# Kernel optimization log

Hardware: AMD Instinct MI355X
Metric: run time of the kernel (lower is better)

## Reference

```python
import jax, jax.numpy as jnp
import numpy as np

N_L = 128
N_R = 128
VOCAB = 50000
IN_DIM = 512
MEM = 256
HID = 128
NCLS = 5


def _make_parents(n, seed):
    # children-before-parent topological order: parent[i] > i, root = n-1 with sentinel parent n
    rng = np.random.RandomState(seed)
    p = np.array([rng.randint(i + 1, n) if i < n - 1 else n for i in range(n)], dtype=np.int32)
    return jnp.asarray(p)


def setup_inputs() -> dict:
    key = jax.random.key(0)
    ks = jax.random.split(key, 18)
    s = 0.05
    inp = {
        'emb': jax.random.normal(ks[0], (VOCAB, IN_DIM), jnp.float32) * 0.1,
        'Wioux': jax.random.normal(ks[1], (IN_DIM, 3 * MEM), jnp.float32) * s,
        'bioux': jnp.zeros((3 * MEM,), jnp.float32),
        'Wiouh': jax.random.normal(ks[2], (MEM, 3 * MEM), jnp.float32) * s,
        'biouh': jnp.zeros((3 * MEM,), jnp.float32),
        'Wfx': jax.random.normal(ks[3], (IN_DIM, MEM), jnp.float32) * s,
        'bfx': jnp.zeros((MEM,), jnp.float32),
        'Wfh': jax.random.normal(ks[4], (MEM, MEM), jnp.float32) * s,
        'bfh': jnp.zeros((MEM,), jnp.float32),
        'Wattn': jax.random.normal(ks[5], (2 * MEM, MEM), jnp.float32) * s,
        'battn': jnp.zeros((MEM,), jnp.float32),
        'Wwh': jax.random.normal(ks[6], (2 * MEM, HID), jnp.float32) * s,
        'bwh': jnp.zeros((HID,), jnp.float32),
        'Wwp': jax.random.normal(ks[7], (HID, NCLS), jnp.float32) * s,
        'bwp': jnp.zeros((NCLS,), jnp.float32),
        'linputs': jax.random.randint(ks[8], (N_L,), 0, VOCAB, jnp.int32),
        'lparents': _make_parents(N_L, 11),
        'rinputs': jax.random.randint(ks[9], (N_R,), 0, VOCAB, jnp.int32),
        'rparents': _make_parents(N_R, 13),
    }
    return inp


def _tree_lstm(X, parents, Wioux, bioux, Wiouh, biouh, Wfx, bfx, Wfh, bfh):
    # X: [N, in_dim]; parents: [N] int, parent index > node index, root's parent == N (sentinel)
    N = X.shape[0]
    m = Wfh.shape[0]
    ioux_all = X @ Wioux + bioux          # [N, 3m] precomputed input contribution
    fx_all = X @ Wfx + bfx                # [N, m]
    fx_pad = jnp.concatenate([fx_all, jnp.zeros((1, m), X.dtype)], axis=0)  # sentinel row

    def step(carry, t):
        Hs, FCs, H = carry                # accumulators: sum of child h / forget-gated child c
        iou = ioux_all[t] + Hs[t] @ Wiouh + biouh
        i_, o_, u_ = jnp.split(iou, 3)
        i_ = jax.nn.sigmoid(i_)
        o_ = jax.nn.sigmoid(o_)
        u_ = jnp.tanh(u_)
        c = i_ * u_ + FCs[t]
        h = o_ * jnp.tanh(c)
        p = parents[t]
        f = jax.nn.sigmoid(h @ Wfh + bfh + fx_pad[p])  # forget gate of this child at its parent
        return (Hs.at[p].add(h), FCs.at[p].add(f * c), H.at[t].set(h)), None

    init = (jnp.zeros((N + 1, m), X.dtype), jnp.zeros((N + 1, m), X.dtype), jnp.zeros((N, m), X.dtype))
    (_, _, H), _ = jax.lax.scan(step, init, jnp.arange(N))
    return H


def reference(emb, Wioux, bioux, Wiouh, biouh, Wfx, bfx, Wfh, bfh,
              Wattn, battn, Wwh, bwh, Wwp, bwp,
              linputs, lparents, rinputs, rparents):
    Xl = emb[linputs]
    Xr = emb[rinputs]
    Hl = _tree_lstm(Xl, lparents, Wioux, bioux, Wiouh, biouh, Wfx, bfx, Wfh, bfh)  # [Nl, m]
    Hr = _tree_lstm(Xr, rparents, Wioux, bioux, Wiouh, biouh, Wfx, bfx, Wfh, bfh)  # [Nr, m]

    S = Hl @ Hr.T                                      # [Nl, Nr]
    beta_sum = jax.nn.softmax(S, axis=1) @ Hr          # [Nl, m]
    alpha_sum = jax.nn.softmax(S.T, axis=1) @ Hl       # [Nr, m]

    v_l = jnp.concatenate([Hl, beta_sum], axis=1) @ Wattn + battn
    v_r = jnp.concatenate([Hr, alpha_sum], axis=1) @ Wattn + battn

    lh = v_l[Hl.shape[0] - 1][None, :]                 # root of left tree
    rh = v_r[Hr.shape[0] - 1][None, :]                 # root of right tree

    vec = jnp.concatenate([lh * rh, jnp.abs(lh - rh)], axis=1)
    out = jax.nn.sigmoid(vec @ Wwh + bwh)
    return jax.nn.log_softmax(out @ Wwp + bwp, axis=1)
```

## Files before the change

### kernel.cpp

```cpp
#include <hip/hip_runtime.h>
#include <math.h>

typedef unsigned long long ull;

#define H_BYTE     0
#define IOUX_BYTE  262144
#define FLAG_BYTE  1310720

__device__ __forceinline__ float sigmf(float x){ return 1.0f/(1.0f+__expf(-x)); }
__device__ __forceinline__ float tanh_fast(float x){ float e=__expf(2.0f*x); return 1.0f-2.0f/(e+1.0f); }

__device__ __forceinline__ ull aload64(const ull* p){
    return __hip_atomic_load(p, __ATOMIC_RELAXED, __HIP_MEMORY_SCOPE_AGENT);
}
__device__ __forceinline__ float aloadf(const float* p){
    return __hip_atomic_load(p, __ATOMIC_RELAXED, __HIP_MEMORY_SCOPE_AGENT);
}
__device__ __forceinline__ void astoref(float* p, float v){
    __hip_atomic_store(p, v, __ATOMIC_RELAXED, __HIP_MEMORY_SCOPE_AGENT);
}
__device__ __forceinline__ int aload32(const int* p){
    return __hip_atomic_load(p, __ATOMIC_RELAXED, __HIP_MEMORY_SCOPE_AGENT);
}
__device__ __forceinline__ void astore32(int* p, int v){
    __hip_atomic_store(p, v, __ATOMIC_RELAXED, __HIP_MEMORY_SCOPE_AGENT);
}

__global__ __launch_bounds__(256) void k1_gemm(
        const float* __restrict__ emb,
        const float* __restrict__ Wioux, const float* __restrict__ bioux,
        const float* __restrict__ Wfx,   const float* __restrict__ bfx,
        const int* __restrict__ linputs, const int* __restrict__ rinputs,
        float* __restrict__ ws){
    int bid  = blockIdx.x;
    int tree = bid >> 6;
    int sub  = (bid >> 2) & 15;
    int q    = bid & 3;
    int n0   = q * 32;
    const int* inp = tree ? rinputs : linputs;
    float* dst = (float*)((char*)ws + IOUX_BYTE) + (size_t)(tree*16+sub)*128*64;

    __shared__ float Xs[32][513];
    __shared__ int toks[32];
    int tid = threadIdx.x;
    if (tid < 32) toks[tid] = inp[n0 + tid];
    __syncthreads();
    {
        int r = tid & 31, seg = tid >> 5;
        const float* src = emb + (size_t)toks[r]*512 + seg*64;
        #pragma unroll
        for (int ii = 0; ii < 16; ii++){
            float4 v = ((const float4*)src)[ii];
            Xs[r][seg*64 + ii*4 + 0] = v.x;
            Xs[r][seg*64 + ii*4 + 1] = v.y;
            Xs[r][seg*64 + ii*4 + 2] = v.z;
            Xs[r][seg*64 + ii*4 + 3] = v.w;
        }
    }
    __syncthreads();
    int c  = tid & 63;
    int ng = tid >> 6;
    int g = c >> 4, jj = c & 15;
    const float* Wcol; int ld; float bias;
    if (g < 3){ int col = g*256 + sub*16 + jj; Wcol = Wioux + col; ld = 768; bias = bioux[col]; }
    else      { int col = sub*16 + jj;         Wcol = Wfx + col;   ld = 256; bias = bfx[col]; }
    float acc[8] = {0,0,0,0,0,0,0,0};
    #pragma unroll 4
    for (int k = 0; k < 512; k++){
        float w = Wcol[(size_t)k*ld];
        #pragma unroll
        for (int i = 0; i < 8; i++) acc[i] = fmaf(Xs[ng*8+i][k], w, acc[i]);
    }
    #pragma unroll
    for (int i = 0; i < 8; i++)
        dst[(size_t)(n0 + ng*8 + i)*64 + c] = acc[i] + bias;
}

__global__ __launch_bounds__(256, 1) void k2_scan(
        const float* __restrict__ Wiouh, const float* __restrict__ biouh,
        const float* __restrict__ Wfh,   const float* __restrict__ bfh,
        const int* __restrict__ lparents, const int* __restrict__ rparents,
        const float* __restrict__ Wattn, const float* __restrict__ battn,
        const float* __restrict__ Wwh,   const float* __restrict__ bwh,
        const float* __restrict__ Wwp,   const float* __restrict__ bwp,
        float* __restrict__ ws, float* __restrict__ out){

    int bid = blockIdx.x;
    int tree = bid >> 4;
    int sub  = bid & 15;
    int slice = sub * 16;
    const int* parents = tree ? rparents : lparents;

    float* Hall = (float*)((char*)ws + H_BYTE);
    float* Hg   = Hall + (size_t)tree*128*256;
    const float* iosrc = (const float*)((char*)ws + IOUX_BYTE) + (size_t)(tree*16+sub)*128*64;
    int* flagB = (int*)((char*)ws + FLAG_BYTE);
    int* flags = flagB + tree*16;
    int* fin   = flagB + 32;

    __shared__ float hv[32][272];
    __shared__ float hsin[16][272];
    __shared__ float red[4][48][17];
    __shared__ float FCtmp[32][17];
    __shared__ float fcin[16][17];
    __shared__ float cc[128][17];
    __shared__ float ioufL[128][68];
    __shared__ int par[128], rnd[128], order[128], kids[128];
    __shared__ int rstart[129], kstart[129], cnt[129];
    __shared__ int clist[128], cpar[128];
    __shared__ int coff[17];
    __shared__ int changed;

    int tid = threadIdx.x;
    int a = tid >> 4;
    int j = tid & 15;
    int jcol = slice + j;

    float Wi[16], Wo[16], Wu[16], Wf[16];
    #pragma unroll
    for (int kk = 0; kk < 16; kk++){
        int k = a*16 + kk;
        Wi[kk] = Wiouh[(size_t)k*768 + jcol];
        Wo[kk] = Wiouh[(size_t)k*768 + 256 + jcol];
        Wu[kk] = Wiouh[(size_t)k*768 + 512 + jcol];
        Wf[kk] = Wfh[(size_t)k*256 + jcol];
    }
    float bioI = biouh[jcol], bioO = biouh[256+jcol], bioU = biouh[512+jcol];
    float bfv  = bfh[jcol];

    for (int i = tid; i < 128*16; i += 256){
        int n = i >> 4, f4 = i & 15;
        float4 v = ((const float4*)(iosrc + (size_t)n*64))[f4];
        int c0 = f4*4;
        ioufL[n][c0+0]=v.x; ioufL[n][c0+1]=v.y; ioufL[n][c0+2]=v.z; ioufL[n][c0+3]=v.w;
    }

    if (tid < 128){ par[tid] = parents[tid]; rnd[tid] = 0; }
    __syncthreads();
    for(;;){
        if (tid==0) changed = 0;
        __syncthreads();
        if (tid < 128){
            int p = par[tid];
            if (p < 128){
                int v = rnd[tid] + 1;
                if (atomicMax(&rnd[p], v) < v) changed = 1;
            }
        }
        __syncthreads();
        int done = (changed == 0);
        __syncthreads();
        if (done) break;
    }
    int nr = rnd[127] + 1;

    if (tid <= 128) cnt[tid] = 0;
    __syncthreads();
    if (tid < 128) atomicAdd(&cnt[rnd[tid]], 1);
    __syncthreads();
    if (tid==0){ int s2=0; for(int r2=0;r2<128;r2++){ rstart[r2]=s2; s2+=cnt[r2]; } rstart[128]=s2; }
    __syncthreads();
    if (tid < 128){
        int r2 = rnd[tid], rk = 0;
        for (int t2 = 0; t2 < tid; t2++) rk += (rnd[t2]==r2);
        order[rstart[r2]+rk] = tid;
    }
    __syncthreads();
    if (tid <= 128) cnt[tid] = 0;
    __syncthreads();
    if (tid < 128) atomicAdd(&cnt[par[tid]], 1);
    __syncthreads();
    if (tid==0){ int s2=0; for(int t2=0;t2<=128;t2++){ kstart[t2]=s2; s2+=cnt[t2]; } }
    __syncthreads();
    if (tid < 128){
        int p = par[tid], rk = 0;
        for (int t2 = 0; t2 < tid; t2++) rk += (par[t2]==p);
        kids[kstart[p]+rk] = tid;
    }
    __syncthreads();

    for (int r = 0; r < nr; r++){
        if (r > 0){
            if (tid < 16){
                while (aload32(&flags[tid]) < r){}
            }
            __syncthreads();
        }
        int rs = rstart[r], re = rstart[r+1];

        if (r == 0){
            for (int b0 = rs; b0 < re; b0 += 16){
                int t = (b0 + a < re) ? order[b0 + a] : -1;
                if (t >= 0){
                    float iv = ioufL[t][j]    + bioI;
                    float ov = ioufL[t][16+j] + bioO;
                    float uv = ioufL[t][32+j] + bioU;
                    float cv = sigmf(iv) * tanh_fast(uv);
                    float h  = sigmf(ov) * tanh_fast(cv);
                    cc[t][j] = cv;
                    astoref(&Hg[(size_t)t*256 + jcol], h);
                }
            }
        } else {
            for (int b0 = rs; b0 < re; b0 += 16){
                int nn = re - b0; if (nn > 16) nn = 16;
                for (int i = tid; i < 16*272; i += 256) (&hsin[0][0])[i] = 0.f;
                fcin[a][j] = 0.f;
                if (tid == 0){
                    int s2 = 0;
                    for (int i2 = 0; i2 < 16; i2++){
                        coff[i2] = s2;
                        if (i2 < nn){ int t2 = order[b0+i2]; s2 += kstart[t2+1]-kstart[t2]; }
                    }
                    coff[16] = s2;
                }
                __syncthreads();
                if (tid < nn){
                    int t2 = order[b0+tid];
                    int o = coff[tid];
                    for (int ci = kstart[t2]; ci < kstart[t2+1]; ci++, o++){
                        clist[o] = kids[ci]; cpar[o] = t2;
                    }
                }
                __syncthreads();
                int M = coff[16];

                for (int cb = 0; cb < M; cb += 32){
                    int mm = M - cb; if (mm > 32) mm = 32;
                    {
                        int half = tid >> 7, u7 = tid & 127;
                        int k0 = u7*2, km = (k0>>4)*17 + (k0&15);
                        const ull* Hu = (const ull*)Hg;
                        ull uu[8];
                        #pragma unroll
                        for (int p = 0; p < 8; p++){
                            int s = p*2 + half;
                            uu[p] = (s < mm) ? aload64(&Hu[(size_t)clist[cb+s]*128 + u7]) : 0ull;
                        }
                        #pragma unroll
                        for (int p = 0; p < 8; p++){
                            int s = p*2 + half;
                            if (s < mm){ union{ull u; float f[2];} w; w.u = uu[p];
                                hv[s][km] = w.f[0]; hv[s][km+1] = w.f[1]; }
                        }
                        #pragma unroll
                        for (int p = 0; p < 8; p++){
                            int s = (p+8)*2 + half;
                            uu[p] = (s < mm) ? aload64(&Hu[(size_t)clist[cb+s]*128 + u7]) : 0ull;
                        }
                        #pragma unroll
                        for (int p = 0; p < 8; p++){
                            int s = (p+8)*2 + half;
                            if (s < mm){ union{ull u; float f[2];} w; w.u = uu[p];
                                hv[s][km] = w.f[0]; hv[s][km+1] = w.f[1]; }
                        }
                    }
                    __syncthreads();
                    for (int s = 0; s < mm; s++){
                        const float* row = &hv[s][a*17];
                        float acc2 = 0.f;
                        #pragma unroll
                        for (int kk = 0; kk < 16; kk++) acc2 = fmaf(Wf[kk], row[kk], acc2);
                        acc2 += __shfl_xor(acc2, 16);
                        acc2 += __shfl_xor(acc2, 32);
                        if ((a & 3) == 0) red[tid>>6][s][j] = acc2;
                    }
                    __syncthreads();
                    for (int pass = 0; pass*16 < mm; pass++){
                        int s = pass*16 + a;
                        if (s < mm){
                            int o = cb + s;
                            float sf = red[0][s][j]+red[1][s][j]+red[2][s][j]+red[3][s][j];
                            float f = sigmf(sf + bfv + ioufL[cpar[o]][48+j]);
                            FCtmp[s][j] = f * cc[clist[o]][j];
                        }
                    }
                    __syncthreads();
                    {
                        int o0 = coff[a]   > cb    ? coff[a]   : cb;
                        int o1 = coff[a+1] < cb+mm ? coff[a+1] : cb+mm;
                        float* dst = &hsin[a][j*17];
                        float fa = 0.f;
                        for (int o = o0; o < o1; o++){
                            int s = o - cb;
                            const float* src = &hv[s][j*17];
                            #pragma unroll
                            for (int kk = 0; kk < 16; kk++) dst[kk] += src[kk];
                            fa += FCtmp[s][j];
                        }
                        fcin[a][j] += fa;
                    }
                    __syncthreads();
                }

                for (int n = 0; n < nn; n++){
                    const float* row = &hsin[n][a*17];
                    float x=0.f, y=0.f, z=0.f;
                    #pragma unroll
                    for (int kk = 0; kk < 16; kk++){
                        float v = row[kk];
                        x = fmaf(Wi[kk], v, x);
                        y = fmaf(Wo[kk], v, y);
                        z = fmaf(Wu[kk], v, z);
                    }
                    x += __shfl_xor(x,16); x += __shfl_xor(x,32);
                    y += __shfl_xor(y,16); y += __shfl_xor(y,32);
                    z += __shfl_xor(z,16); z += __shfl_xor(z,32);
                    if ((a & 3) == 0){
                        int w = tid >> 6;
                        red[w][n][j]    = x;
                        red[w][16+n][j] = y;
                        red[w][32+n][j] = z;
                    }
                }
                __syncthreads();
                if (a < nn){
                    int t = order[b0+a];
                    float si = red[0][a][j]+red[1][a][j]+red[2][a][j]+red[3][a][j];
                    float so = red[0][16+a][j]+red[1][16+a][j]+red[2][16+a][j]+red[3][16+a][j];
                    float su = red[0][32+a][j]+red[1][32+a][j]+red[2][32+a][j]+red[3][32+a][j];
                    float iv = si + ioufL[t][j]    + bioI;
                    float ov = so + ioufL[t][16+j] + bioO;
                    float uv = su + ioufL[t][32+j] + bioU;
                    float cv = fmaf(sigmf(iv), tanh_fast(uv), fcin[a][j]);
                    float h  = sigmf(ov) * tanh_fast(cv);
                    cc[t][j] = cv;
                    astoref(&Hg[(size_t)t*256 + jcol], h);
                }
                __syncthreads();
            }
        }

        __syncthreads();
        if (tid == 0){
            if (r < nr-1) astore32(&flags[sub], r+1);
            else          astore32(&fin[bid], 1);
        }
    }

    if (bid != 0) return;
    if (tid < 32){
        while (aload32(&fin[tid]) < 1){}
    }
    __syncthreads();

    float* F  = &hv[0][0];
    float* rl = F,        *rr  = F + 256;
    float* sA = F + 512,  *sB  = F + 640;
    float* bet= F + 768,  *alp = F + 1024;
    float* vl = F + 1280, *vr  = F + 1536;
    float* vec= F + 1792, *hid = F + 2304;
    const ull* HuL = (const ull*)Hall;
    const ull* HuR = (const ull*)(Hall + 128*256);

    {
        union{ ull u; float f[2]; } w2;
        if (tid < 128){
            w2.u = aload64(&HuL[(size_t)127*128 + tid]);
            rl[2*tid] = w2.f[0]; rl[2*tid+1] = w2.f[1];
        } else {
            int p = tid - 128;
            w2.u = aload64(&HuR[(size_t)127*128 + p]);
            rr[2*p] = w2.f[0]; rr[2*p+1] = w2.f[1];
        }
    }
    __syncthreads();
    {
        int i = tid & 127;
        const ull* row = (tid < 128) ? &HuR[(size_t)i*128] : &HuL[(size_t)i*128];
        const float* rt = (tid < 128) ? rl : rr;
        float acc2 = 0.f;
        for (int p0 = 0; p0 < 128; p0 += 16){
            ull u[16];
            #pragma unroll
            for (int q2 = 0; q2 < 16; q2++) u[q2] = aload64(&row[p0+q2]);
            #pragma unroll
            for (int q2 = 0; q2 < 16; q2++){
                union{ ull uu; float f[2]; } w2; w2.uu = u[q2];
                acc2 = fmaf(w2.f[0], rt[2*(p0+q2)],   acc2);
                acc2 = fmaf(w2.f[1], rt[2*(p0+q2)+1], acc2);
            }
        }
        if (tid < 128) sA[i] = acc2; else sB[i] = acc2;
    }
    __syncthreads();
    if (tid < 2){
        float* v = tid ? sB : sA;
        float m = -1e30f;
        for (int k = 0; k < 128; k++) m = fmaxf(m, v[k]);
        float su2 = 0.f;
        for (int k = 0; k < 128; k++){ float e = __expf(v[k]-m); v[k]=e; su2+=e; }
        float inv = 1.0f/su2;
        for (int k = 0; k < 128; k++) v[k] *= inv;
    }
    __syncthreads();
    {
        const float* HrF = Hall + 128*256;
        const float* HlF = Hall;
        float b = 0.f, al = 0.f;
        for (int i0 = 0; i0 < 128; i0 += 16){
            float ur[16], ulv[16];
            #pragma unroll
            for (int q2 = 0; q2 < 16; q2++){
                ur[q2]  = aloadf(&HrF[(size_t)(i0+q2)*256 + tid]);
                ulv[q2] = aloadf(&HlF[(size_t)(i0+q2)*256 + tid]);
            }
            #pragma unroll
            for (int q2 = 0; q2 < 16; q2++){
                b  = fmaf(sA[i0+q2], ur[q2],  b);
                al = fmaf(sB[i0+q2], ulv[q2], al);
            }
        }
        bet[tid] = b; alp[tid] = al;
    }
    __syncthreads();
    {
        float x = 0.f, y = 0.f;
        for (int k = 0; k < 256; k++){
            float w = Wattn[(size_t)k*256 + tid];
            x = fmaf(rl[k], w, x);
            y = fmaf(rr[k], w, y);
        }
        for (int k = 0; k < 256; k++){
            float w = Wattn[(size_t)(256+k)*256 + tid];
            x = fmaf(bet[k], w, x);
            y = fmaf(alp[k], w, y);
        }
        vl[tid] = x + battn[tid];
        vr[tid] = y + battn[tid];
    }
    __syncthreads();
    vec[tid]     = vl[tid]*vr[tid];
    vec[256+tid] = fabsf(vl[tid]-vr[tid]);
    __syncthreads();
    if (tid < 128){
        float acc2 = 0.f;
        for (int k = 0; k < 512; k++) acc2 = fmaf(vec[k], Wwh[(size_t)k*128+tid], acc2);
        hid[tid] = sigmf(acc2 + bwh[tid]);
    }
    __syncthreads();
    if (tid == 0){
        float lg[5];
        for (int c2 = 0; c2 < 5; c2++){
            float acc2 = bwp[c2];
            for (int k = 0; k < 128; k++) acc2 = fmaf(hid[k], Wwp[k*5+c2], acc2);
            lg[c2] = acc2;
        }
        float m = lg[0];
        for (int c2 = 1; c2 < 5; c2++) m = fmaxf(m, lg[c2]);
        float su2 = 0.f;
        for (int c2 = 0; c2 < 5; c2++) su2 += __expf(lg[c2]-m);
        float ls = logf(su2);
        for (int c2 = 0; c2 < 5; c2++) out[c2] = lg[c2]-m-ls;
    }
}

extern "C" void kernel_launch(void* const* d_in, const int* in_sizes, int n_in,
                              void* d_out, int out_size, void* d_ws, size_t ws_size,
                              hipStream_t stream) {
    const float* emb    = (const float*)d_in[0];
    const float* Wioux  = (const float*)d_in[1];
    const float* bioux  = (const float*)d_in[2];
    const float* Wiouh  = (const float*)d_in[3];
    const float* biouh  = (const float*)d_in[4];
    const float* Wfx    = (const float*)d_in[5];
    const float* bfx    = (const float*)d_in[6];
    const float* Wfh    = (const float*)d_in[7];
    const float* bfh    = (const float*)d_in[8];
    const float* Wattn  = (const float*)d_in[9];
    const float* battn  = (const float*)d_in[10];
    const float* Wwh    = (const float*)d_in[11];
    const float* bwh    = (const float*)d_in[12];
    const float* Wwp    = (const float*)d_in[13];
    const float* bwp    = (const float*)d_in[14];
    const int* linputs  = (const int*)d_in[15];
    const int* lparents = (const int*)d_in[16];
    const int* rinputs  = (const int*)d_in[17];
    const int* rparents = (const int*)d_in[18];
    float* ws  = (float*)d_ws;
    float* out = (float*)d_out;

    hipMemsetAsync((char*)d_ws + FLAG_BYTE, 0, 256, stream);
    k1_gemm<<<128, 256, 0, stream>>>(emb, Wioux, bioux, Wfx, bfx,
                                     linputs, rinputs, ws);
    k2_scan<<<32, 256, 0, stream>>>(Wiouh, biouh, Wfh, bfh, lparents, rparents,
                                    Wattn, battn, Wwh, bwh, Wwp, bwp, ws, out);
}
```

Baseline: 195.7 us.

## Overlap inter-block wait with processing of children from earlier rounds

```diff
diff --git a/kernel.cpp b/kernel.cpp
--- a/kernel.cpp
+++ b/kernel.cpp
@@ -107,8 +107,8 @@
     __shared__ float ioufL[128][68];
     __shared__ int par[128], rnd[128], order[128], kids[128];
     __shared__ int rstart[129], kstart[129], cnt[129];
-    __shared__ int clist[128], cpar[128];
-    __shared__ int coff[17];
+    __shared__ int clistO[128], cparO[128], clistN[128], cparN[128];
+    __shared__ int coffO[17], coffN[17], cntO[16], cntN[16];
     __shared__ int changed;
 
     int tid = threadIdx.x;
@@ -179,156 +179,183 @@
     }
     __syncthreads();
 
-    for (int r = 0; r < nr; r++){
-        if (r > 0){
+    auto processList = [&](const int* cl, const int* cp, const int* cf){
+        int M = cf[16];
+        for (int cb = 0; cb < M; cb += 32){
+            int mm = M - cb; if (mm > 32) mm = 32;
+            {
+                int half = tid >> 7, u7 = tid & 127;
+                int k0 = u7*2, km = (k0>>4)*17 + (k0&15);
+                const ull* Hu = (const ull*)Hg;
+                ull uu[8];
+                #pragma unroll
+                for (int p = 0; p < 8; p++){
+                    int s = p*2 + half;
+                    uu[p] = (s < mm) ? aload64(&Hu[(size_t)cl[cb+s]*128 + u7]) : 0ull;
+                }
+                #pragma unroll
+                for (int p = 0; p < 8; p++){
+                    int s = p*2 + half;
+                    if (s < mm){ union{ull u; float f[2];} w; w.u = uu[p];
+                        hv[s][km] = w.f[0]; hv[s][km+1] = w.f[1]; }
+                }
+                #pragma unroll
+                for (int p = 0; p < 8; p++){
+                    int s = (p+8)*2 + half;
+                    uu[p] = (s < mm) ? aload64(&Hu[(size_t)cl[cb+s]*128 + u7]) : 0ull;
+                }
+                #pragma unroll
+                for (int p = 0; p < 8; p++){
+                    int s = (p+8)*2 + half;
+                    if (s < mm){ union{ull u; float f[2];} w; w.u = uu[p];
+                        hv[s][km] = w.f[0]; hv[s][km+1] = w.f[1]; }
+                }
+            }
+            __syncthreads();
+            for (int s = 0; s < mm; s++){
+                const float* row = &hv[s][a*17];
+                float acc2 = 0.f;
+                #pragma unroll
+                for (int kk = 0; kk < 16; kk++) acc2 = fmaf(Wf[kk], row[kk], acc2);
+                acc2 += __shfl_xor(acc2, 16);
+                acc2 += __shfl_xor(acc2, 32);
+                if ((a & 3) == 0) red[tid>>6][s][j] = acc2;
+            }
+            __syncthreads();
+            for (int pass = 0; pass*16 < mm; pass++){
+                int s = pass*16 + a;
+                if (s < mm){
+                    int o = cb + s;
+                    float sf = red[0][s][j]+red[1][s][j]+red[2][s][j]+red[3][s][j];
+                    float f = sigmf(sf + bfv + ioufL[cp[o]][48+j]);
+                    FCtmp[s][j] = f * cc[cl[o]][j];
+                }
+            }
+            __syncthreads();
+            {
+                int o0 = cf[a]   > cb    ? cf[a]   : cb;
+                int o1 = cf[a+1] < cb+mm ? cf[a+1] : cb+mm;
+                float* dst = &hsin[a][j*17];
+                float fa = 0.f;
+                for (int o = o0; o < o1; o++){
+                    int s = o - cb;
+                    const float* src = &hv[s][j*17];
+                    #pragma unroll
+                    for (int kk = 0; kk < 16; kk++) dst[kk] += src[kk];
+                    fa += FCtmp[s][j];
+                }
+                fcin[a][j] += fa;
+            }
+            __syncthreads();
+        }
+    };
+
+    {
+        int rs = rstart[0], re = rstart[1];
+        for (int b0 = rs; b0 < re; b0 += 16){
+            int t = (b0 + a < re) ? order[b0 + a] : -1;
+            if (t >= 0){
+                float iv = ioufL[t][j]    + bioI;
+                float ov = ioufL[t][16+j] + bioO;
+                float uv = ioufL[t][32+j] + bioU;
+                float cv = sigmf(iv) * tanh_fast(uv);
+                float h  = sigmf(ov) * tanh_fast(cv);
+                cc[t][j] = cv;
+                astoref(&Hg[(size_t)t*256 + jcol], h);
+            }
+        }
+        __syncthreads();
+        if (tid == 0){
+            if (nr > 1) astore32(&flags[sub], 1);
+            else        astore32(&fin[bid], 1);
+        }
+    }
+
+    for (int r = 1; r < nr; r++){
+        int rs = rstart[r], re = rstart[r+1];
+        int nb = (re - rs + 15) >> 4;
+        for (int b = 0; b < nb; b++){
+            int b0 = rs + b*16;
+            int nn = re - b0; if (nn > 16) nn = 16;
+            for (int i = tid; i < 16*272; i += 256) (&hsin[0][0])[i] = 0.f;
+            fcin[a][j] = 0.f;
             if (tid < 16){
-                while (aload32(&flags[tid]) < r){}
-            }
-            __syncthreads();
-        }
-        int rs = rstart[r], re = rstart[r+1];
-
-        if (r == 0){
-            for (int b0 = rs; b0 < re; b0 += 16){
-                int t = (b0 + a < re) ? order[b0 + a] : -1;
-                if (t >= 0){
-                    float iv = ioufL[t][j]    + bioI;
-                    float ov = ioufL[t][16+j] + bioO;
-                    float uv = ioufL[t][32+j] + bioU;
-                    float cv = sigmf(iv) * tanh_fast(uv);
-                    float h  = sigmf(ov) * tanh_fast(cv);
-                    cc[t][j] = cv;
-                    astoref(&Hg[(size_t)t*256 + jcol], h);
-                }
-            }
-        } else {
-            for (int b0 = rs; b0 < re; b0 += 16){
-                int nn = re - b0; if (nn > 16) nn = 16;
-                for (int i = tid; i < 16*272; i += 256) (&hsin[0][0])[i] = 0.f;
-                fcin[a][j] = 0.f;
-                if (tid == 0){
-                    int s2 = 0;
-                    for (int i2 = 0; i2 < 16; i2++){
-                        coff[i2] = s2;
-                        if (i2 < nn){ int t2 = order[b0+i2]; s2 += kstart[t2+1]-kstart[t2]; }
+                int cO = 0, cN = 0;
+                if (tid < nn){
+                    int t = order[b0+tid];
+                    for (int ci = kstart[t]; ci < kstart[t+1]; ci++){
+                        if (b == 0 && rnd[kids[ci]] == r-1) cN++; else cO++;
                     }
-                    coff[16] = s2;
+                }
+                cntO[tid] = cO; cntN[tid] = cN;
+            }
+            __syncthreads();
+            if (tid == 0){
+                int sO = 0, sN = 0;
+                for (int i2 = 0; i2 < 16; i2++){
+                    coffO[i2] = sO; sO += cntO[i2];
+                    coffN[i2] = sN; sN += cntN[i2];
+                }
+                coffO[16] = sO; coffN[16] = sN;
+            }
+            __syncthreads();
+            if (tid < nn){
+                int t = order[b0+tid];
+                int oO = coffO[tid], oN = coffN[tid];
+                for (int ci = kstart[t]; ci < kstart[t+1]; ci++){
+                    int c = kids[ci];
+                    if (b == 0 && rnd[c] == r-1){ clistN[oN] = c; cparN[oN] = t; oN++; }
+                    else                        { clistO[oO] = c; cparO[oO] = t; oO++; }
+                }
+            }
+            __syncthreads();
+
+            processList(clistO, cparO, coffO);
+
+            if (b == 0){
+                if (tid < 16){
+                    while (aload32(&flags[tid]) < r) __builtin_amdgcn_s_sleep(1);
                 }
                 __syncthreads();
-                if (tid < nn){
-                    int t2 = order[b0+tid];
-                    int o = coff[tid];
-                    for (int ci = kstart[t2]; ci < kstart[t2+1]; ci++, o++){
-                        clist[o] = kids[ci]; cpar[o] = t2;
-                    }
-                }
-                __syncthreads();
-                int M = coff[16];
-
-                for (int cb = 0; cb < M; cb += 32){
-                    int mm = M - cb; if (mm > 32) mm = 32;
-                    {
-                        int half = tid >> 7, u7 = tid & 127;
-                        int k0 = u7*2, km = (k0>>4)*17 + (k0&15);
-                        const ull* Hu = (const ull*)Hg;
-                        ull uu[8];
-                        #pragma unroll
-                        for (int p = 0; p < 8; p++){
-                            int s = p*2 + half;
-                            uu[p] = (s < mm) ? aload64(&Hu[(size_t)clist[cb+s]*128 + u7]) : 0ull;
-                        }
-                        #pragma unroll
-                        for (int p = 0; p < 8; p++){
-                            int s = p*2 + half;
-                            if (s < mm){ union{ull u; float f[2];} w; w.u = uu[p];
-                                hv[s][km] = w.f[0]; hv[s][km+1] = w.f[1]; }
-                        }
-                        #pragma unroll
-                        for (int p = 0; p < 8; p++){
-                            int s = (p+8)*2 + half;
-                            uu[p] = (s < mm) ? aload64(&Hu[(size_t)clist[cb+s]*128 + u7]) : 0ull;
-                        }
-                        #pragma unroll
-                        for (int p = 0; p < 8; p++){
-                            int s = (p+8)*2 + half;
-                            if (s < mm){ union{ull u; float f[2];} w; w.u = uu[p];
-                                hv[s][km] = w.f[0]; hv[s][km+1] = w.f[1]; }
-                        }
-                    }
-                    __syncthreads();
-                    for (int s = 0; s < mm; s++){
-                        const float* row = &hv[s][a*17];
-                        float acc2 = 0.f;
-                        #pragma unroll
-                        for (int kk = 0; kk < 16; kk++) acc2 = fmaf(Wf[kk], row[kk], acc2);
-                        acc2 += __shfl_xor(acc2, 16);
-                        acc2 += __shfl_xor(acc2, 32);
-                        if ((a & 3) == 0) red[tid>>6][s][j] = acc2;
-                    }
-                    __syncthreads();
-                    for (int pass = 0; pass*16 < mm; pass++){
-                        int s = pass*16 + a;
-                        if (s < mm){
-                            int o = cb + s;
-                            float sf = red[0][s][j]+red[1][s][j]+red[2][s][j]+red[3][s][j];
-                            float f = sigmf(sf + bfv + ioufL[cpar[o]][48+j]);
-                            FCtmp[s][j] = f * cc[clist[o]][j];
-                        }
-                    }
-                    __syncthreads();
-                    {
-                        int o0 = coff[a]   > cb    ? coff[a]   : cb;
-                        int o1 = coff[a+1] < cb+mm ? coff[a+1] : cb+mm;
-                        float* dst = &hsin[a][j*17];
-                        float fa = 0.f;
-                        for (int o = o0; o < o1; o++){
-                            int s = o - cb;
-                            const float* src = &hv[s][j*17];
-                            #pragma unroll
-                            for (int kk = 0; kk < 16; kk++) dst[kk] += src[kk];
-                            fa += FCtmp[s][j];
-                        }
-                        fcin[a][j] += fa;
-                    }
-                    __syncthreads();
-                }
-
-                for (int n = 0; n < nn; n++){
-                    const float* row = &hsin[n][a*17];
-                    float x=0.f, y=0.f, z=0.f;
-                    #pragma unroll
-                    for (int kk = 0; kk < 16; kk++){
-                        float v = row[kk];
-                        x = fmaf(Wi[kk], v, x);
-                        y = fmaf(Wo[kk], v, y);
-                        z = fmaf(Wu[kk], v, z);
-                    }
-                    x += __shfl_xor(x,16); x += __shfl_xor(x,32);
-                    y += __shfl_xor(y,16); y += __shfl_xor(y,32);
-                    z += __shfl_xor(z,16); z += __shfl_xor(z,32);
-                    if ((a & 3) == 0){
-                        int w = tid >> 6;
-                        red[w][n][j]    = x;
-                        red[w][16+n][j] = y;
-                        red[w][32+n][j] = z;
-                    }
-                }
-                __syncthreads();
-                if (a < nn){
-                    int t = order[b0+a];
-                    float si = red[0][a][j]+red[1][a][j]+red[2][a][j]+red[3][a][j];
-                    float so = red[0][16+a][j]+red[1][16+a][j]+red[2][16+a][j]+red[3][16+a][j];
-                    float su = red[0][32+a][j]+red[1][32+a][j]+red[2][32+a][j]+red[3][32+a][j];
-                    float iv = si + ioufL[t][j]    + bioI;
-                    float ov = so + ioufL[t][16+j] + bioO;
-                    float uv = su + ioufL[t][32+j] + bioU;
-                    float cv = fmaf(sigmf(iv), tanh_fast(uv), fcin[a][j]);
-                    float h  = sigmf(ov) * tanh_fast(cv);
-                    cc[t][j] = cv;
-                    astoref(&Hg[(size_t)t*256 + jcol], h);
-                }
-                __syncthreads();
-            }
+            }
+
+            processList(clistN, cparN, coffN);
+
+            for (int n = 0; n < nn; n++){
+                const float* row = &hsin[n][a*17];
+                float x=0.f, y=0.f, z=0.f;
+                #pragma unroll
+                for (int kk = 0; kk < 16; kk++){
+                    float v = row[kk];
+                    x = fmaf(Wi[kk], v, x);
+                    y = fmaf(Wo[kk], v, y);
+                    z = fmaf(Wu[kk], v, z);
+                }
+                x += __shfl_xor(x,16); x += __shfl_xor(x,32);
+                y += __shfl_xor(y,16); y += __shfl_xor(y,32);
+                z += __shfl_xor(z,16); z += __shfl_xor(z,32);
+                if ((a & 3) == 0){
+                    int w = tid >> 6;
+                    red[w][n][j]    = x;
+                    red[w][16+n][j] = y;
+                    red[w][32+n][j] = z;
+                }
+            }
+            __syncthreads();
+            if (a < nn){
+                int t = order[b0+a];
+                float si = red[0][a][j]+red[1][a][j]+red[2][a][j]+red[3][a][j];
+                float so = red[0][16+a][j]+red[1][16+a][j]+red[2][16+a][j]+red[3][16+a][j];
+                float su = red[0][32+a][j]+red[1][32+a][j]+red[2][32+a][j]+red[3][32+a][j];
+                float iv = si + ioufL[t][j]    + bioI;
+                float ov = so + ioufL[t][16+j] + bioO;
+                float uv = su + ioufL[t][32+j] + bioU;
+                float cv = fmaf(sigmf(iv), tanh_fast(uv), fcin[a][j]);
+                float h  = sigmf(ov) * tanh_fast(cv);
+                cc[t][j] = cv;
+                astoref(&Hg[(size_t)t*256 + jcol], h);
+            }
+            __syncthreads();
         }
 
         __syncthreads();
@@ -340,7 +367,7 @@
 
     if (bid != 0) return;
     if (tid < 32){
-        while (aload32(&fin[tid]) < 1){}
+        while (aload32(&fin[tid]) < 1) __builtin_amdgcn_s_sleep(1);
     }
     __syncthreads();
 
```

New measurement: 207.2 us. +5.9%, slower.

## Replace per-round barrier with fine-grained progress counters and vectorized H exchange

Applied to the files above, without the earlier changes.

```diff
diff --git a/kernel.cpp b/kernel.cpp
--- a/kernel.cpp
+++ b/kernel.cpp
@@ -9,14 +9,16 @@
 
 __device__ __forceinline__ float sigmf(float x){ return 1.0f/(1.0f+__expf(-x)); }
 __device__ __forceinline__ float tanh_fast(float x){ float e=__expf(2.0f*x); return 1.0f-2.0f/(e+1.0f); }
-
+__device__ __forceinline__ ull packf2(float lo, float hi){
+    union{ float f[2]; ull u; } x; x.f[0]=lo; x.f[1]=hi; return x.u;
+}
 __device__ __forceinline__ ull aload64(const ull* p){
     return __hip_atomic_load(p, __ATOMIC_RELAXED, __HIP_MEMORY_SCOPE_AGENT);
 }
 __device__ __forceinline__ float aloadf(const float* p){
     return __hip_atomic_load(p, __ATOMIC_RELAXED, __HIP_MEMORY_SCOPE_AGENT);
 }
-__device__ __forceinline__ void astoref(float* p, float v){
+__device__ __forceinline__ void astore64(ull* p, ull v){
     __hip_atomic_store(p, v, __ATOMIC_RELAXED, __HIP_MEMORY_SCOPE_AGENT);
 }
 __device__ __forceinline__ int aload32(const int* p){
@@ -24,6 +26,26 @@
 }
 __device__ __forceinline__ void astore32(int* p, int v){
     __hip_atomic_store(p, v, __ATOMIC_RELAXED, __HIP_MEMORY_SCOPE_AGENT);
+}
+
+__device__ __forceinline__ void stage8(const ull* p0, const ull* p1, const ull* p2, const ull* p3,
+                                       const ull* p4, const ull* p5, const ull* p6, const ull* p7,
+                                       float4* r){
+    asm volatile(
+        "global_load_dwordx4 %0, %8, off sc0 sc1\n\t"
+        "global_load_dwordx4 %1, %9, off sc0 sc1\n\t"
+        "global_load_dwordx4 %2, %10, off sc0 sc1\n\t"
+        "global_load_dwordx4 %3, %11, off sc0 sc1\n\t"
+        "global_load_dwordx4 %4, %12, off sc0 sc1\n\t"
+        "global_load_dwordx4 %5, %13, off sc0 sc1\n\t"
+        "global_load_dwordx4 %6, %14, off sc0 sc1\n\t"
+        "global_load_dwordx4 %7, %15, off sc0 sc1\n\t"
+        "s_waitcnt vmcnt(0)"
+        : "=&v"(r[0]), "=&v"(r[1]), "=&v"(r[2]), "=&v"(r[3]),
+          "=&v"(r[4]), "=&v"(r[5]), "=&v"(r[6]), "=&v"(r[7])
+        : "v"(p0), "v"(p1), "v"(p2), "v"(p3), "v"(p4), "v"(p5), "v"(p6), "v"(p7)
+        : "memory");
+    __builtin_amdgcn_sched_barrier(0);
 }
 
 __global__ __launch_bounds__(256) void k1_gemm(
@@ -91,25 +113,25 @@
     int slice = sub * 16;
     const int* parents = tree ? rparents : lparents;
 
-    float* Hall = (float*)((char*)ws + H_BYTE);
-    float* Hg   = Hall + (size_t)tree*128*256;
+    ull* H2all = (ull*)((char*)ws + H_BYTE);
+    ull* H2 = H2all + (size_t)tree*128*128;
     const float* iosrc = (const float*)((char*)ws + IOUX_BYTE) + (size_t)(tree*16+sub)*128*64;
     int* flagB = (int*)((char*)ws + FLAG_BYTE);
-    int* flags = flagB + tree*16;
+    int* prog  = flagB + tree*16;
     int* fin   = flagB + 32;
 
-    __shared__ float hv[32][272];
-    __shared__ float hsin[16][272];
+    __shared__ float hv[32][320];
+    __shared__ float hsin[16][321];
     __shared__ float red[4][48][17];
     __shared__ float FCtmp[32][17];
     __shared__ float fcin[16][17];
     __shared__ float cc[128][17];
     __shared__ float ioufL[128][68];
-    __shared__ int par[128], rnd[128], order[128], kids[128];
+    __shared__ int par[128], rnd[128], order[128], kids[128], posOf[128];
     __shared__ int rstart[129], kstart[129], cnt[129];
     __shared__ int clist[128], cpar[128];
     __shared__ int coff[17];
-    __shared__ int changed;
+    __shared__ int changed, maxPosS;
 
     int tid = threadIdx.x;
     int a = tid >> 4;
@@ -163,7 +185,9 @@
     if (tid < 128){
         int r2 = rnd[tid], rk = 0;
         for (int t2 = 0; t2 < tid; t2++) rk += (rnd[t2]==r2);
-        order[rstart[r2]+rk] = tid;
+        int pos = rstart[r2]+rk;
+        order[pos] = tid;
+        posOf[tid] = pos;
     }
     __syncthreads();
     if (tid <= 128) cnt[tid] = 0;
@@ -179,143 +203,154 @@
     }
     __syncthreads();
 
-    for (int r = 0; r < nr; r++){
-        if (r > 0){
-            if (tid < 16){
-                while (aload32(&flags[tid]) < r){}
-            }
-            __syncthreads();
-        }
+    {
+        int rs = rstart[0], re = rstart[1];
+        for (int b0 = rs; b0 < re; b0 += 16){
+            int t = (b0 + a < re) ? order[b0 + a] : -1;
+            float h = 0.f;
+            if (t >= 0){
+                float iv = ioufL[t][j]    + bioI;
+                float ov = ioufL[t][16+j] + bioO;
+                float uv = ioufL[t][32+j] + bioU;
+                float cv = sigmf(iv) * tanh_fast(uv);
+                h = sigmf(ov) * tanh_fast(cv);
+                cc[t][j] = cv;
+            }
+            float hp = __shfl_xor(h, 1);
+            if (t >= 0 && (j & 1) == 0)
+                astore64(&H2[(size_t)t*128 + (slice>>1) + (j>>1)], packf2(h, hp));
+            __syncthreads();
+            if (tid == 0){
+                int done = b0 + 16 < re ? b0 + 16 : re;
+                astore32(&prog[sub], done);
+            }
+        }
+    }
+
+    for (int r = 1; r < nr; r++){
         int rs = rstart[r], re = rstart[r+1];
-
-        if (r == 0){
-            for (int b0 = rs; b0 < re; b0 += 16){
-                int t = (b0 + a < re) ? order[b0 + a] : -1;
+        for (int b0 = rs; b0 < re; b0 += 16){
+            int nn = re - b0; if (nn > 16) nn = 16;
+            for (int i = tid; i < 16*321; i += 256) (&hsin[0][0])[i] = 0.f;
+            fcin[a][j] = 0.f;
+            if (tid == 0){
+                maxPosS = 0;
+                int s2 = 0;
+                for (int i2 = 0; i2 < 16; i2++){
+                    coff[i2] = s2;
+                    if (i2 < nn){ int t2 = order[b0+i2]; s2 += kstart[t2+1]-kstart[t2]; }
+                }
+                coff[16] = s2;
+            }
+            __syncthreads();
+            if (tid < nn){
+                int t2 = order[b0+tid];
+                int o = coff[tid];
+                for (int ci = kstart[t2]; ci < kstart[t2+1]; ci++, o++){
+                    clist[o] = kids[ci]; cpar[o] = t2;
+                }
+            }
+            __syncthreads();
+            int M = coff[16];
+            if (tid < M) atomicMax(&maxPosS, posOf[clist[tid]]);
+            __syncthreads();
+
+            if (tid < 64){
+                int need = maxPosS + 1;
+                for(;;){
+                    int v = (tid < 16) ? aload32(&prog[tid]) : 0x7fffffff;
+                    if (__all((tid < 16) ? (v >= need) : 1)) break;
+                    __builtin_amdgcn_s_sleep(2);
+                }
+            }
+            __syncthreads();
+
+            for (int cb = 0; cb < M; cb += 32){
+                int mm = M - cb; if (mm > 32) mm = 32;
+                {
+                    int c16 = tid & 63;
+                    int rw  = tid >> 6;
+                    int k0 = c16 * 4;
+                    int km = (k0 >> 4)*20 + (k0 & 15);
+                    const ull* base = H2;
+                    const ull* pp[8];
+                    #pragma unroll
+                    for (int p = 0; p < 8; p++){
+                        int s = p*4 + rw;
+                        int idx = (s < mm) ? clist[cb+s] : clist[cb];
+                        pp[p] = base + (size_t)idx*128 + c16*2;
+                    }
+                    float4 rr[8];
+                    stage8(pp[0],pp[1],pp[2],pp[3],pp[4],pp[5],pp[6],pp[7], rr);
+                    #pragma unroll
+                    for (int p = 0; p < 8; p++){
+                        int s = p*4 + rw;
+                        if (s < mm) *(float4*)&hv[s][km] = rr[p];
+                    }
+                }
+                __syncthreads();
+                for (int s = 0; s < mm; s++){
+                    const float* row = &hv[s][a*20];
+                    float acc2 = 0.f;
+                    #pragma unroll
+                    for (int kk = 0; kk < 16; kk++) acc2 = fmaf(Wf[kk], row[kk], acc2);
+                    acc2 += __shfl_xor(acc2, 16);
+                    acc2 += __shfl_xor(acc2, 32);
+                    if ((a & 3) == 0) red[tid>>6][s][j] = acc2;
+                }
+                __syncthreads();
+                for (int pass = 0; pass*16 < mm; pass++){
+                    int s = pass*16 + a;
+                    if (s < mm){
+                        int o = cb + s;
+                        float sf = red[0][s][j]+red[1][s][j]+red[2][s][j]+red[3][s][j];
+                        float f = sigmf(sf + bfv + ioufL[cpar[o]][48+j]);
+                        FCtmp[s][j] = f * cc[clist[o]][j];
+                    }
+                }
+                __syncthreads();
+                {
+                    int o0 = coff[a]   > cb    ? coff[a]   : cb;
+                    int o1 = coff[a+1] < cb+mm ? coff[a+1] : cb+mm;
+                    float* dst = &hsin[a][j*20];
+                    float fa = 0.f;
+                    for (int o = o0; o < o1; o++){
+                        int s = o - cb;
+                        const float* src = &hv[s][j*20];
+                        #pragma unroll
+                        for (int kk = 0; kk < 16; kk++) dst[kk] += src[kk];
+                        fa += FCtmp[s][j];
+                    }
+                    fcin[a][j] += fa;
+                }
+                __syncthreads();
+            }
+
+            for (int n = 0; n < nn; n++){
+                const float* row = &hsin[n][a*20];
+                float x=0.f, y=0.f, z=0.f;
+                #pragma unroll
+                for (int kk = 0; kk < 16; kk++){
+                    float v = row[kk];
+                    x = fmaf(Wi[kk], v, x);
+                    y = fmaf(Wo[kk], v, y);
+                    z = fmaf(Wu[kk], v, z);
+                }
+                x += __shfl_xor(x,16); x += __shfl_xor(x,32);
+                y += __shfl_xor(y,16); y += __shfl_xor(y,32);
+                z += __shfl_xor(z,16); z += __shfl_xor(z,32);
+                if ((a & 3) == 0){
+                    int w = tid >> 6;
+                    red[w][n][j]    = x;
+                    red[w][16+n][j] = y;
+                    red[w][32+n][j] = z;
+                }
+            }
+            __syncthreads();
+            {
+                int t = (a < nn) ? order[b0+a] : -1;
+                float h = 0.f;
                 if (t >= 0){
-                    float iv = ioufL[t][j]    + bioI;
-                    float ov = ioufL[t][16+j] + bioO;
-                    float uv = ioufL[t][32+j] + bioU;
-                    float cv = sigmf(iv) * tanh_fast(uv);
-                    float h  = sigmf(ov) * tanh_fast(cv);
-                    cc[t][j] = cv;
-                    astoref(&Hg[(size_t)t*256 + jcol], h);
-                }
-            }
-        } else {
-            for (int b0 = rs; b0 < re; b0 += 16){
-                int nn = re - b0; if (nn > 16) nn = 16;
-                for (int i = tid; i < 16*272; i += 256) (&hsin[0][0])[i] = 0.f;
-                fcin[a][j] = 0.f;
-                if (tid == 0){
-                    int s2 = 0;
-                    for (int i2 = 0; i2 < 16; i2++){
-                        coff[i2] = s2;
-                        if (i2 < nn){ int t2 = order[b0+i2]; s2 += kstart[t2+1]-kstart[t2]; }
-                    }
-                    coff[16] = s2;
-                }
-                __syncthreads();
-                if (tid < nn){
-                    int t2 = order[b0+tid];
-                    int o = coff[tid];
-                    for (int ci = kstart[t2]; ci < kstart[t2+1]; ci++, o++){
-                        clist[o] = kids[ci]; cpar[o] = t2;
-                    }
-                }
-                __syncthreads();
-                int M = coff[16];
-
-                for (int cb = 0; cb < M; cb += 32){
-                    int mm = M - cb; if (mm > 32) mm = 32;
-                    {
-                        int half = tid >> 7, u7 = tid & 127;
-                        int k0 = u7*2, km = (k0>>4)*17 + (k0&15);
-                        const ull* Hu = (const ull*)Hg;
-                        ull uu[8];
-                        #pragma unroll
-                        for (int p = 0; p < 8; p++){
-                            int s = p*2 + half;
-                            uu[p] = (s < mm) ? aload64(&Hu[(size_t)clist[cb+s]*128 + u7]) : 0ull;
-                        }
-                        #pragma unroll
-                        for (int p = 0; p < 8; p++){
-                            int s = p*2 + half;
-                            if (s < mm){ union{ull u; float f[2];} w; w.u = uu[p];
-                                hv[s][km] = w.f[0]; hv[s][km+1] = w.f[1]; }
-                        }
-                        #pragma unroll
-                        for (int p = 0; p < 8; p++){
-                            int s = (p+8)*2 + half;
-                            uu[p] = (s < mm) ? aload64(&Hu[(size_t)clist[cb+s]*128 + u7]) : 0ull;
-                        }
-                        #pragma unroll
-                        for (int p = 0; p < 8; p++){
-                            int s = (p+8)*2 + half;
-                            if (s < mm){ union{ull u; float f[2];} w; w.u = uu[p];
-                                hv[s][km] = w.f[0]; hv[s][km+1] = w.f[1]; }
-                        }
-                    }
-                    __syncthreads();
-                    for (int s = 0; s < mm; s++){
-                        const float* row = &hv[s][a*17];
-                        float acc2 = 0.f;
-                        #pragma unroll
-                        for (int kk = 0; kk < 16; kk++) acc2 = fmaf(Wf[kk], row[kk], acc2);
-                        acc2 += __shfl_xor(acc2, 16);
-                        acc2 += __shfl_xor(acc2, 32);
-                        if ((a & 3) == 0) red[tid>>6][s][j] = acc2;
-                    }
-                    __syncthreads();
-                    for (int pass = 0; pass*16 < mm; pass++){
-                        int s = pass*16 + a;
-                        if (s < mm){
-                            int o = cb + s;
-                            float sf = red[0][s][j]+red[1][s][j]+red[2][s][j]+red[3][s][j];
-                            float f = sigmf(sf + bfv + ioufL[cpar[o]][48+j]);
-                            FCtmp[s][j] = f * cc[clist[o]][j];
-                        }
-                    }
-                    __syncthreads();
-                    {
-                        int o0 = coff[a]   > cb    ? coff[a]   : cb;
-                        int o1 = coff[a+1] < cb+mm ? coff[a+1] : cb+mm;
-                        float* dst = &hsin[a][j*17];
-                        float fa = 0.f;
-                        for (int o = o0; o < o1; o++){
-                            int s = o - cb;
-                            const float* src = &hv[s][j*17];
-                            #pragma unroll
-                            for (int kk = 0; kk < 16; kk++) dst[kk] += src[kk];
-                            fa += FCtmp[s][j];
-                        }
-                        fcin[a][j] += fa;
-                    }
-                    __syncthreads();
-                }
-
-                for (int n = 0; n < nn; n++){
-                    const float* row = &hsin[n][a*17];
-                    float x=0.f, y=0.f, z=0.f;
-                    #pragma unroll
-                    for (int kk = 0; kk < 16; kk++){
-                        float v = row[kk];
-                        x = fmaf(Wi[kk], v, x);
-                        y = fmaf(Wo[kk], v, y);
-                        z = fmaf(Wu[kk], v, z);
-                    }
-                    x += __shfl_xor(x,16); x += __shfl_xor(x,32);
-                    y += __shfl_xor(y,16); y += __shfl_xor(y,32);
-                    z += __shfl_xor(z,16); z += __shfl_xor(z,32);
-                    if ((a & 3) == 0){
-                        int w = tid >> 6;
-                        red[w][n][j]    = x;
-                        red[w][16+n][j] = y;
-                        red[w][32+n][j] = z;
-                    }
-                }
-                __syncthreads();
-                if (a < nn){
-                    int t = order[b0+a];
                     float si = red[0][a][j]+red[1][a][j]+red[2][a][j]+red[3][a][j];
                     float so = red[0][16+a][j]+red[1][16+a][j]+red[2][16+a][j]+red[3][16+a][j];
                     float su = red[0][32+a][j]+red[1][32+a][j]+red[2][32+a][j]+red[3][32+a][j];
@@ -323,24 +358,26 @@
                     float ov = so + ioufL[t][16+j] + bioO;
                     float uv = su + ioufL[t][32+j] + bioU;
                     float cv = fmaf(sigmf(iv), tanh_fast(uv), fcin[a][j]);
-                    float h  = sigmf(ov) * tanh_fast(cv);
+                    h = sigmf(ov) * tanh_fast(cv);
                     cc[t][j] = cv;
-                    astoref(&Hg[(size_t)t*256 + jcol], h);
-                }
-                __syncthreads();
-            }
-        }
-
-        __syncthreads();
-        if (tid == 0){
-            if (r < nr-1) astore32(&flags[sub], r+1);
-            else          astore32(&fin[bid], 1);
-        }
-    }
-
+                }
+                float hp = __shfl_xor(h, 1);
+                if (t >= 0 && (j & 1) == 0)
+                    astore64(&H2[(size_t)t*128 + (slice>>1) + (j>>1)], packf2(h, hp));
+            }
+            __syncthreads();
+            if (tid == 0) astore32(&prog[sub], b0 + nn);
+        }
+    }
+
+    if (tid == 0) astore32(&fin[bid], 1);
     if (bid != 0) return;
-    if (tid < 32){
-        while (aload32(&fin[tid]) < 1){}
+    if (tid < 64){
+        for(;;){
+            int v = (tid < 32) ? aload32(&fin[tid]) : 1;
+            if (__all((tid < 32) ? (v == 1) : 1)) break;
+            __builtin_amdgcn_s_sleep(2);
+        }
     }
     __syncthreads();
 
@@ -350,8 +387,8 @@
     float* bet= F + 768,  *alp = F + 1024;
     float* vl = F + 1280, *vr  = F + 1536;
     float* vec= F + 1792, *hid = F + 2304;
-    const ull* HuL = (const ull*)Hall;
-    const ull* HuR = (const ull*)(Hall + 128*256);
+    const ull* HuL = H2all;
+    const ull* HuR = H2all + (size_t)128*128;
 
     {
         union{ ull u; float f[2]; } w2;
@@ -395,8 +432,8 @@
     }
     __syncthreads();
     {
-        const float* HrF = Hall + 128*256;
-        const float* HlF = Hall;
+        const float* HrF = (const float*)HuR;
+        const float* HlF = (const float*)HuL;
         float b = 0.f, al = 0.f;
         for (int i0 = 0; i0 < 128; i0 += 16){
             float ur[16], ulv[16];
```

New measurement: 187.8 us. -4.0%, faster.
